# Kernel tuning notes

Hardware: AMD Instinct MI355X
Metric: run time of the kernel (lower is better)

The kernel has to match this reference:

```python
import jax, jax.numpy as jnp
import numpy as np

B, IN, H, T = 512, 256, 128, 100

def _build_norm_adj():
    # Hardcoded topology from GraphConvLSTM.build_graph (22 nodes, cliques per sublist)
    adj_list = [[0, 2, 5, 8, 11], [0, 1, 4, 7, 10], [0, 3, 6, 9, 12, 15],
                [9, 14, 17, 19, 21], [9, 13, 16, 18, 20]]
    n = max(max(s) for s in adj_list) + 1  # 22
    A = np.zeros((n, n), dtype=np.float32)
    for s in adj_list:
        for i in range(len(s)):
            for j in range(i + 1, len(s)):
                A[s[i], s[j]] = 1.0
                A[s[j], s[i]] = 1.0
    # DGL GraphConv norm='both': D^{-1/2} A D^{-1/2} (degrees clamped to >=1)
    deg = np.clip(A.sum(axis=1), 1.0, None)
    dinv = 1.0 / np.sqrt(deg)
    return jnp.asarray(dinv[:, None] * A * dinv[None, :])  # (N, N)

A_NORM = _build_norm_adj()
N = A_NORM.shape[0]  # 22

def setup_inputs() -> dict:
    key = jax.random.key(0)
    ks = jax.random.split(key, 11)
    s_in = 1.0 / np.sqrt(IN)
    s_h = 1.0 / np.sqrt(H)
    return {
        "x":     jax.random.normal(ks[0], (B, IN), jnp.float32),
        "wi_w":  jax.random.normal(ks[1], (H, IN), jnp.float32) * s_in,
        "wi_b":  jax.random.normal(ks[2], (H,), jnp.float32) * s_in,
        "wf_w":  jax.random.normal(ks[3], (H, IN), jnp.float32) * s_in,
        "wf_b":  jax.random.normal(ks[4], (H,), jnp.float32) * s_in,
        "wo_w":  jax.random.normal(ks[5], (H, IN), jnp.float32) * s_in,
        "wo_b":  jax.random.normal(ks[6], (H,), jnp.float32) * s_in,
        "wc_w":  jax.random.normal(ks[7], (H, IN), jnp.float32) * s_in,
        "wc_b":  jax.random.normal(ks[8], (H,), jnp.float32) * s_in,
        "gcn_w": jax.random.normal(ks[9], (H, H), jnp.float32) * s_h,
        "gcn_b": jax.random.normal(ks[10], (H,), jnp.float32) * s_h,
    }

def reference(x, wi_w, wi_b, wf_w, wf_b, wo_w, wo_b, wc_w, wc_b, gcn_w, gcn_b):
    # x is fixed across timesteps in the original forward -> project gates once.
    xi = (x @ wi_w.T + wi_b)[:, None, :]  # (B,1,H) broadcast over nodes
    xf = (x @ wf_w.T + wf_b)[:, None, :]
    xo = (x @ wo_w.T + wo_b)[:, None, :]
    xc = (x @ wc_w.T + wc_b)[:, None, :]

    def step(carry, _):
        h, c = carry
        # All four gates share the identical gcn_h(g, h_prev) result.
        msg = jnp.einsum('mn,bnh->bmh', A_NORM, h)  # (B,N,H)
        g = msg @ gcn_w + gcn_b
        i_t = jax.nn.sigmoid(xi + g)
        f_t = jax.nn.sigmoid(xf + g)
        o_t = jax.nn.sigmoid(xo + g)
        c_til = jnp.tanh(xc + g)
        c_t = f_t * c + i_t * c_til
        h_t = o_t * jnp.tanh(c_t)
        return (h_t, c_t), h_t

    h0 = jnp.zeros((B, N, H), x.dtype)
    c0 = jnp.zeros((B, N, H), x.dtype)
    _, hs = jax.lax.scan(step, (h0, c0), None, length=T)  # (T,B,N,H)
    out = jnp.transpose(hs, (1, 0, 2, 3)).reshape(B, -1)  # (B, T*N*H)
    return out
```

## Files before the change

### kernel.cpp

```cpp
#include <hip/hip_runtime.h>
#include <hip/hip_bf16.h>
#include <math.h>


#define B_   512
#define IN_  256
#define H_   128
#define T_   100
#define N_   22
#define NH   (N_ * H_)
#define TNH  (T_ * NH)
#define HP   136
#define THREADS 512
#define LOG2E 1.442695041f

typedef __attribute__((ext_vector_type(8)))  _Float16 half8_t;
typedef __attribute__((ext_vector_type(16))) float    f32x16;

__global__ void __launch_bounds__(THREADS, 4)
gclstm_kernel(const float* __restrict__ x,
              const float* __restrict__ wi_w, const float* __restrict__ wi_b,
              const float* __restrict__ wf_w, const float* __restrict__ wf_b,
              const float* __restrict__ wo_w, const float* __restrict__ wo_b,
              const float* __restrict__ wc_w, const float* __restrict__ wc_b,
              const float* __restrict__ gcn_w, const float* __restrict__ gcn_b,
              float* __restrict__ out)
{
    __shared__ __align__(16) _Float16 h_hi[32][HP];
    __shared__ __align__(16) _Float16 h_lo[32][HP];
    __shared__ __align__(16) float    hw_T[H_ * 32];
    __shared__ float xp_lds[4][H_];
    __shared__ __align__(16) float xrow[IN_];

    const int t     = threadIdx.x;
    const int b     = blockIdx.x;
    const int ho    = t & (H_ - 1);
    const int mg    = t >> 7;
    const int wid   = t >> 6;
    const int lane  = t & 63;
    const int l31   = lane & 31;
    const int khalf = lane >> 5;

    if (t < IN_ / 4) {
        reinterpret_cast<float4*>(xrow)[t] =
            reinterpret_cast<const float4*>(x + (size_t)b * IN_)[t];
    }
    for (int e = t; e < 32 * HP / 2; e += THREADS) ((int*)h_hi)[e] = 0;
    for (int e = t; e < 32 * HP / 2; e += THREADS) ((int*)h_lo)[e] = 0;
    __syncthreads();

    {
        const float* wg = (mg == 0) ? wi_w : (mg == 1) ? wf_w : (mg == 2) ? wo_w : wc_w;
        const float* bg = (mg == 0) ? wi_b : (mg == 1) ? wf_b : (mg == 2) ? wo_b : wc_b;
        const float* rg = wg + (size_t)ho * IN_;
        float acc = bg[ho];
        #pragma unroll
        for (int k4 = 0; k4 < IN_ / 4; ++k4) {
            float4 xv = reinterpret_cast<const float4*>(xrow)[k4];
            float4 wv = reinterpret_cast<const float4*>(rg)[k4];
            acc += wv.x * xv.x + wv.y * xv.y + wv.z * xv.z + wv.w * xv.w;
        }
        xp_lds[mg][ho] = acc;
    }

    half8_t Bf[8];
    if (wid < 4) {
        const int col = 32 * wid + l31;
        #pragma unroll
        for (int kk = 0; kk < 8; ++kk) {
            #pragma unroll
            for (int i = 0; i < 8; ++i) {
                Bf[kk][i] = (_Float16)gcn_w[(16 * kk + 8 * khalf + i) * H_ + col];
            }
        }
    }
    __syncthreads();

    const float gb   = gcn_b[ho];
    const float xi_r = xp_lds[0][ho] + gb;
    const float xf_r = xp_lds[1][ho] + gb;
    const float xo_r = xp_lds[2][ho] + gb;
    const float xc_r = xp_lds[3][ho] + gb;
    const float Ei   = __builtin_exp2f(-LOG2E * xi_r);
    const float Ef   = __builtin_exp2f(-LOG2E * xf_r);
    const float Eo   = __builtin_exp2f(-LOG2E * xo_r);
    const float E2c  = __builtin_exp2f(-2.0f * LOG2E * xc_r);

    float c_reg[6];
    #pragma unroll
    for (int i = 0; i < 6; ++i) c_reg[i] = 0.0f;

    float* outb = out + (size_t)b * TNH + ho;

    #define D13 0.2773500981126146f
    #define D5  0.4472135954999579f
    #define D4  0.5f
    const float DINV[22] = {D13, D4, D4, D5, D4, D4, D5, D4, D4, D13, D4,
                            D4,  D5, D4, D4, D5, D4, D4, D4, D4, D4,  D4};

    for (int step = 0; step < T_; ++step) {
        if (wid < 4) {
            f32x16 acc = (f32x16)(0.0f);
            #pragma unroll
            for (int kk = 0; kk < 8; ++kk) {
                const int ko = 16 * kk + 8 * khalf;
                const half8_t Ah = *reinterpret_cast<const half8_t*>(&h_hi[l31][ko]);
                const half8_t Al = *reinterpret_cast<const half8_t*>(&h_lo[l31][ko]);
                acc = __builtin_amdgcn_mfma_f32_32x32x16_f16(Ah, Bf[kk], acc, 0, 0, 0);
                acc = __builtin_amdgcn_mfma_f32_32x32x16_f16(Al, Bf[kk], acc, 0, 0, 0);
            }
            const int col = 32 * wid + l31;
            #pragma unroll
            for (int q = 0; q < 4; ++q) {
                float4 v = make_float4(acc[4 * q], acc[4 * q + 1],
                                       acc[4 * q + 2], acc[4 * q + 3]);
                const int unit = (2 * q + khalf) ^ (col & 7);
                *reinterpret_cast<float4*>(&hw_T[col * 32 + unit * 4]) = v;
            }
        }
        __syncthreads();

        float tt[24];
        #pragma unroll
        for (int u = 0; u < 6; ++u) {
            const int unit = u ^ (ho & 7);
            float4 v = *reinterpret_cast<const float4*>(&hw_T[ho * 32 + unit * 4]);
            tt[4 * u + 0] = v.x; tt[4 * u + 1] = v.y;
            tt[4 * u + 2] = v.z; tt[4 * u + 3] = v.w;
        }
        #pragma unroll
        for (int m = 0; m < 22; ++m) tt[m] *= DINV[m];

        const float S0 = tt[0] + tt[2] + tt[5] + tt[8] + tt[11];
        const float S1 = tt[0] + tt[1] + tt[4] + tt[7] + tt[10];
        const float S2 = tt[0] + tt[3] + tt[6] + tt[9] + tt[12] + tt[15];
        const float S3 = tt[9] + tt[14] + tt[17] + tt[19] + tt[21];
        const float S4 = tt[9] + tt[13] + tt[16] + tt[18] + tt[20];

        float* outs = outb + (size_t)step * NH;

        #define UPD(n, nn, SSexpr, KK) {                                        \
            const float g   = DINV[n] * ((SSexpr) - (KK) * tt[n]);              \
            const float E   = __builtin_exp2f(-LOG2E * g);                      \
            const float it  = __builtin_amdgcn_rcpf(1.0f + E * Ei);             \
            const float ft  = __builtin_amdgcn_rcpf(1.0f + E * Ef);             \
            const float ot  = __builtin_amdgcn_rcpf(1.0f + E * Eo);             \
            const float e2  = fminf(E * E * E2c, 1e30f);                        \
            const float ct  = (1.0f - e2) * __builtin_amdgcn_rcpf(1.0f + e2);   \
            const float cn  = ft * c_reg[nn] + it * ct;                         \
            c_reg[nn] = cn;                                                     \
            const float e2n = fminf(__builtin_exp2f(-2.0f * LOG2E * cn), 1e30f);\
            const float th  = (1.0f - e2n) * __builtin_amdgcn_rcpf(1.0f + e2n); \
            const float hn  = ot * th;                                          \
            outs[(n) * H_] = hn;                                                \
            const _Float16 hh = (_Float16)hn;                                   \
            h_hi[n][ho] = hh;                                                   \
            h_lo[n][ho] = (_Float16)(hn - (float)hh);                           \
        }

        if (mg == 0) {
            UPD(0, 0, S0 + S1 + S2, 3.0f)
            UPD(1, 1, S1, 1.0f)
            UPD(2, 2, S0, 1.0f)
            UPD(3, 3, S2, 1.0f)
            UPD(4, 4, S1, 1.0f)
            UPD(5, 5, S0, 1.0f)
        } else if (mg == 1) {
            UPD(6, 0, S2, 1.0f)
            UPD(7, 1, S1, 1.0f)
            UPD(8, 2, S0, 1.0f)
            UPD(9, 3, S2 + S3 + S4, 3.0f)
            UPD(10, 4, S1, 1.0f)
        } else if (mg == 2) {
            UPD(11, 0, S0, 1.0f)
            UPD(12, 1, S2, 1.0f)
            UPD(13, 2, S4, 1.0f)
            UPD(14, 3, S3, 1.0f)
            UPD(15, 4, S2, 1.0f)
            UPD(16, 5, S4, 1.0f)
        } else {
            UPD(17, 0, S3, 1.0f)
            UPD(18, 1, S4, 1.0f)
            UPD(19, 2, S3, 1.0f)
            UPD(20, 3, S4, 1.0f)
            UPD(21, 4, S3, 1.0f)
        }
        #undef UPD
        __syncthreads();
    }
}

extern "C" void kernel_launch(void* const* d_in, const int* in_sizes, int n_in,
                              void* d_out, int out_size, void* d_ws, size_t ws_size,
                              hipStream_t stream) {
    const float* x     = (const float*)d_in[0];
    const float* wi_w  = (const float*)d_in[1];
    const float* wi_b  = (const float*)d_in[2];
    const float* wf_w  = (const float*)d_in[3];
    const float* wf_b  = (const float*)d_in[4];
    const float* wo_w  = (const float*)d_in[5];
    const float* wo_b  = (const float*)d_in[6];
    const float* wc_w  = (const float*)d_in[7];
    const float* wc_b  = (const float*)d_in[8];
    const float* gcn_w = (const float*)d_in[9];
    const float* gcn_b = (const float*)d_in[10];
    float* out = (float*)d_out;

    gclstm_kernel<<<dim3(B_), dim3(THREADS), 0, stream>>>(
        x, wi_w, wi_b, wf_w, wf_b, wo_w, wo_b, wc_w, wc_b, gcn_w, gcn_b, out);
}
```

Before: 794.5 us.

## Keep MFMA results in registers and split node updates across half-waves

The block shrinks to 256 threads (four waves), and every wave runs the MFMA for its 32 output columns. The hi and lo products now go into two separate accumulators, which gives the MFMA chain two independent dependency paths. The results are exchanged between half-waves with a cross-lane shuffle instead of the shared-memory transpose buffer, which removes one barrier and the LDS round trip per step. Each lane then updates 11 nodes instead of 5-6, so per-thread serial transcendental work grows and twice as many blocks can share a CU.

```diff
diff --git a/kernel.cpp b/kernel.cpp
--- a/kernel.cpp
+++ b/kernel.cpp
@@ -11,13 +11,17 @@
 #define NH   (N_ * H_)
 #define TNH  (T_ * NH)
 #define HP   136
-#define THREADS 512
+#define THREADS 256
 #define LOG2E 1.442695041f
 
 typedef __attribute__((ext_vector_type(8)))  _Float16 half8_t;
 typedef __attribute__((ext_vector_type(16))) float    f32x16;
 
-__global__ void __launch_bounds__(THREADS, 4)
+#define D13 0.2773500981126146f
+#define D5  0.4472135954999579f
+#define D4  0.5f
+
+__global__ void __launch_bounds__(THREADS, 2)
 gclstm_kernel(const float* __restrict__ x,
               const float* __restrict__ wi_w, const float* __restrict__ wi_b,
               const float* __restrict__ wf_w, const float* __restrict__ wf_b,
@@ -28,18 +32,17 @@
 {
     __shared__ __align__(16) _Float16 h_hi[32][HP];
     __shared__ __align__(16) _Float16 h_lo[32][HP];
-    __shared__ __align__(16) float    hw_T[H_ * 32];
     __shared__ float xp_lds[4][H_];
     __shared__ __align__(16) float xrow[IN_];
 
     const int t     = threadIdx.x;
     const int b     = blockIdx.x;
-    const int ho    = t & (H_ - 1);
-    const int mg    = t >> 7;
+    const int lane  = t & 63;
     const int wid   = t >> 6;
-    const int lane  = t & 63;
     const int l31   = lane & 31;
     const int khalf = lane >> 5;
+    const bool k0   = (khalf == 0);
+    const int col   = 32 * wid + l31;
 
     if (t < IN_ / 4) {
         reinterpret_cast<float4*>(xrow)[t] =
@@ -50,97 +53,102 @@
     __syncthreads();
 
     {
-        const float* wg = (mg == 0) ? wi_w : (mg == 1) ? wf_w : (mg == 2) ? wo_w : wc_w;
-        const float* bg = (mg == 0) ? wi_b : (mg == 1) ? wf_b : (mg == 2) ? wo_b : wc_b;
-        const float* rg = wg + (size_t)ho * IN_;
-        float acc = bg[ho];
+        const int ho2 = t & (H_ - 1);
+        const int mg2 = t >> 7;
+        const float* wA = mg2 ? wf_w : wi_w;  const float* bA = mg2 ? wf_b : wi_b;
+        const float* wB = mg2 ? wc_w : wo_w;  const float* bB = mg2 ? wc_b : wo_b;
+        const float* rA = wA + (size_t)ho2 * IN_;
+        const float* rB = wB + (size_t)ho2 * IN_;
+        float accA = bA[ho2], accB = bB[ho2];
         #pragma unroll
         for (int k4 = 0; k4 < IN_ / 4; ++k4) {
             float4 xv = reinterpret_cast<const float4*>(xrow)[k4];
-            float4 wv = reinterpret_cast<const float4*>(rg)[k4];
-            acc += wv.x * xv.x + wv.y * xv.y + wv.z * xv.z + wv.w * xv.w;
-        }
-        xp_lds[mg][ho] = acc;
+            float4 wv = reinterpret_cast<const float4*>(rA)[k4];
+            accA += wv.x * xv.x + wv.y * xv.y + wv.z * xv.z + wv.w * xv.w;
+            float4 uv = reinterpret_cast<const float4*>(rB)[k4];
+            accB += uv.x * xv.x + uv.y * xv.y + uv.z * xv.z + uv.w * xv.w;
+        }
+        xp_lds[mg2][ho2]     = accA;
+        xp_lds[mg2 + 2][ho2] = accB;
     }
 
     half8_t Bf[8];
-    if (wid < 4) {
-        const int col = 32 * wid + l31;
+    #pragma unroll
+    for (int kk = 0; kk < 8; ++kk) {
+        #pragma unroll
+        for (int i = 0; i < 8; ++i) {
+            Bf[kk][i] = (_Float16)gcn_w[(16 * kk + 8 * khalf + i) * H_ + col];
+        }
+    }
+    __syncthreads();
+
+    const float gb  = gcn_b[col];
+    const float Ei  = __builtin_exp2f(-LOG2E * (xp_lds[0][col] + gb));
+    const float Ef  = __builtin_exp2f(-LOG2E * (xp_lds[1][col] + gb));
+    const float Eo  = __builtin_exp2f(-LOG2E * (xp_lds[2][col] + gb));
+    const float E2c = __builtin_exp2f(-2.0f * LOG2E * (xp_lds[3][col] + gb));
+
+    const float A1_0 = k0 ? D13 : D4;  const float A2_0 = k0 ? 3.0f * D13 : D4;
+    const float A1_1 = k0 ? D4 : D5;
+    const float A1_3 = k0 ? D5 : D4;
+    const float A1_4 = k0 ? D4 : D5;
+    const float A1_6 = k0 ? D5 : D4;
+    const float A1_9 = k0 ? D13 : D4;  const float A2_9 = k0 ? 3.0f * D13 : D4;
+
+    float c_reg[11];
+    #pragma unroll
+    for (int i = 0; i < 11; ++i) c_reg[i] = 0.0f;
+
+    const int nb = k0 ? 0 : 11;
+    _Float16* hhp = &h_hi[0][0] + nb * HP + col;
+    _Float16* hlp = &h_lo[0][0] + nb * HP + col;
+    float* outb = out + (size_t)b * TNH + nb * H_ + col;
+
+    for (int step = 0; step < T_; ++step) {
+        f32x16 accA = (f32x16)(0.0f);
+        f32x16 accB = (f32x16)(0.0f);
         #pragma unroll
         for (int kk = 0; kk < 8; ++kk) {
-            #pragma unroll
-            for (int i = 0; i < 8; ++i) {
-                Bf[kk][i] = (_Float16)gcn_w[(16 * kk + 8 * khalf + i) * H_ + col];
-            }
-        }
-    }
-    __syncthreads();
-
-    const float gb   = gcn_b[ho];
-    const float xi_r = xp_lds[0][ho] + gb;
-    const float xf_r = xp_lds[1][ho] + gb;
-    const float xo_r = xp_lds[2][ho] + gb;
-    const float xc_r = xp_lds[3][ho] + gb;
-    const float Ei   = __builtin_exp2f(-LOG2E * xi_r);
-    const float Ef   = __builtin_exp2f(-LOG2E * xf_r);
-    const float Eo   = __builtin_exp2f(-LOG2E * xo_r);
-    const float E2c  = __builtin_exp2f(-2.0f * LOG2E * xc_r);
-
-    float c_reg[6];
-    #pragma unroll
-    for (int i = 0; i < 6; ++i) c_reg[i] = 0.0f;
-
-    float* outb = out + (size_t)b * TNH + ho;
-
-    #define D13 0.2773500981126146f
-    #define D5  0.4472135954999579f
-    #define D4  0.5f
-    const float DINV[22] = {D13, D4, D4, D5, D4, D4, D5, D4, D4, D13, D4,
-                            D4,  D5, D4, D4, D5, D4, D4, D4, D4, D4,  D4};
-
-    for (int step = 0; step < T_; ++step) {
-        if (wid < 4) {
-            f32x16 acc = (f32x16)(0.0f);
-            #pragma unroll
-            for (int kk = 0; kk < 8; ++kk) {
-                const int ko = 16 * kk + 8 * khalf;
-                const half8_t Ah = *reinterpret_cast<const half8_t*>(&h_hi[l31][ko]);
-                const half8_t Al = *reinterpret_cast<const half8_t*>(&h_lo[l31][ko]);
-                acc = __builtin_amdgcn_mfma_f32_32x32x16_f16(Ah, Bf[kk], acc, 0, 0, 0);
-                acc = __builtin_amdgcn_mfma_f32_32x32x16_f16(Al, Bf[kk], acc, 0, 0, 0);
-            }
-            const int col = 32 * wid + l31;
-            #pragma unroll
-            for (int q = 0; q < 4; ++q) {
-                float4 v = make_float4(acc[4 * q], acc[4 * q + 1],
-                                       acc[4 * q + 2], acc[4 * q + 3]);
-                const int unit = (2 * q + khalf) ^ (col & 7);
-                *reinterpret_cast<float4*>(&hw_T[col * 32 + unit * 4]) = v;
-            }
-        }
-        __syncthreads();
-
-        float tt[24];
-        #pragma unroll
-        for (int u = 0; u < 6; ++u) {
-            const int unit = u ^ (ho & 7);
-            float4 v = *reinterpret_cast<const float4*>(&hw_T[ho * 32 + unit * 4]);
-            tt[4 * u + 0] = v.x; tt[4 * u + 1] = v.y;
-            tt[4 * u + 2] = v.z; tt[4 * u + 3] = v.w;
-        }
-        #pragma unroll
-        for (int m = 0; m < 22; ++m) tt[m] *= DINV[m];
-
-        const float S0 = tt[0] + tt[2] + tt[5] + tt[8] + tt[11];
-        const float S1 = tt[0] + tt[1] + tt[4] + tt[7] + tt[10];
-        const float S2 = tt[0] + tt[3] + tt[6] + tt[9] + tt[12] + tt[15];
-        const float S3 = tt[9] + tt[14] + tt[17] + tt[19] + tt[21];
-        const float S4 = tt[9] + tt[13] + tt[16] + tt[18] + tt[20];
+            const int ko = 16 * kk + 8 * khalf;
+            const half8_t Ah = *reinterpret_cast<const half8_t*>(&h_hi[l31][ko]);
+            const half8_t Al = *reinterpret_cast<const half8_t*>(&h_lo[l31][ko]);
+            accA = __builtin_amdgcn_mfma_f32_32x32x16_f16(Ah, Bf[kk], accA, 0, 0, 0);
+            accB = __builtin_amdgcn_mfma_f32_32x32x16_f16(Al, Bf[kk], accB, 0, 0, 0);
+        }
+        float hw[12];
+        #pragma unroll
+        for (int s = 0; s < 12; ++s) hw[s] = accA[s] + accB[s];
+
+        float oth[12];
+        #pragma unroll
+        for (int s = 0; s < 12; ++s) oth[s] = __shfl_xor(hw[s], 32, 64);
+        float sel0[12], sel1[10];
+        #pragma unroll
+        for (int s = 0; s < 12; ++s) sel0[s] = k0 ? hw[s] : oth[s];
+        #pragma unroll
+        for (int s = 0; s < 10; ++s) sel1[s] = k0 ? oth[s] : hw[s];
+
+        const float tt0  = sel0[0] * D13, tt1  = sel0[1] * D4, tt2  = sel0[2] * D4;
+        const float tt3  = sel0[3] * D5,  tt4  = sel1[0] * D4, tt5  = sel1[1] * D4;
+        const float tt6  = sel1[2] * D5,  tt7  = sel1[3] * D4, tt8  = sel0[4] * D4;
+        const float tt9  = sel0[5] * D13, tt10 = sel0[6] * D4, tt11 = sel0[7] * D4;
+        const float tt12 = sel1[4] * D5,  tt13 = sel1[5] * D4, tt14 = sel1[6] * D4;
+        const float tt15 = sel1[7] * D5,  tt16 = sel0[8] * D4, tt17 = sel0[9] * D4;
+        const float tt18 = sel0[10] * D4, tt19 = sel0[11] * D4;
+        const float tt20 = sel1[8] * D4,  tt21 = sel1[9] * D4;
+
+        const float S0 = tt0 + tt2 + tt5 + tt8 + tt11;
+        const float S1 = tt0 + tt1 + tt4 + tt7 + tt10;
+        const float S2 = tt0 + tt3 + tt6 + tt9 + tt12 + tt15;
+        const float S3 = tt9 + tt14 + tt17 + tt19 + tt21;
+        const float S4 = tt9 + tt13 + tt16 + tt18 + tt20;
+        const float SAB = S0 + S1 + S2;
+        const float SCD = S2 + S3 + S4;
 
         float* outs = outb + (size_t)step * NH;
 
-        #define UPD(n, nn, SSexpr, KK) {                                        \
-            const float g   = DINV[n] * ((SSexpr) - (KK) * tt[n]);              \
+        #define UPD(nn, A1v, A2v, SSv, TMYv) {                                  \
+            const float g   = (A1v) * (SSv) - (A2v) * (TMYv);                   \
             const float E   = __builtin_exp2f(-LOG2E * g);                      \
             const float it  = __builtin_amdgcn_rcpf(1.0f + E * Ei);             \
             const float ft  = __builtin_amdgcn_rcpf(1.0f + E * Ef);             \
@@ -152,40 +160,25 @@
             const float e2n = fminf(__builtin_exp2f(-2.0f * LOG2E * cn), 1e30f);\
             const float th  = (1.0f - e2n) * __builtin_amdgcn_rcpf(1.0f + e2n); \
             const float hn  = ot * th;                                          \
-            outs[(n) * H_] = hn;                                                \
+            outs[(nn) * H_] = hn;                                               \
             const _Float16 hh = (_Float16)hn;                                   \
-            h_hi[n][ho] = hh;                                                   \
-            h_lo[n][ho] = (_Float16)(hn - (float)hh);                           \
-        }
-
-        if (mg == 0) {
-            UPD(0, 0, S0 + S1 + S2, 3.0f)
-            UPD(1, 1, S1, 1.0f)
-            UPD(2, 2, S0, 1.0f)
-            UPD(3, 3, S2, 1.0f)
-            UPD(4, 4, S1, 1.0f)
-            UPD(5, 5, S0, 1.0f)
-        } else if (mg == 1) {
-            UPD(6, 0, S2, 1.0f)
-            UPD(7, 1, S1, 1.0f)
-            UPD(8, 2, S0, 1.0f)
-            UPD(9, 3, S2 + S3 + S4, 3.0f)
-            UPD(10, 4, S1, 1.0f)
-        } else if (mg == 2) {
-            UPD(11, 0, S0, 1.0f)
-            UPD(12, 1, S2, 1.0f)
-            UPD(13, 2, S4, 1.0f)
-            UPD(14, 3, S3, 1.0f)
-            UPD(15, 4, S2, 1.0f)
-            UPD(16, 5, S4, 1.0f)
-        } else {
-            UPD(17, 0, S3, 1.0f)
-            UPD(18, 1, S4, 1.0f)
-            UPD(19, 2, S3, 1.0f)
-            UPD(20, 3, S4, 1.0f)
-            UPD(21, 4, S3, 1.0f)
-        }
+            hhp[(nn) * HP] = hh;                                                \
+            hlp[(nn) * HP] = (_Float16)(hn - (float)hh);                        \
+        }
+
+        UPD(0,  A1_0, A2_0, k0 ? SAB : S0, k0 ? tt0  : tt11)
+        UPD(1,  A1_1, A1_1, k0 ? S1  : S2, k0 ? tt1  : tt12)
+        UPD(2,  D4,   D4,   k0 ? S0  : S4, k0 ? tt2  : tt13)
+        UPD(3,  A1_3, A1_3, k0 ? S2  : S3, k0 ? tt3  : tt14)
+        UPD(4,  A1_4, A1_4, k0 ? S1  : S2, k0 ? tt4  : tt15)
+        UPD(5,  D4,   D4,   k0 ? S0  : S4, k0 ? tt5  : tt16)
+        UPD(6,  A1_6, A1_6, k0 ? S2  : S3, k0 ? tt6  : tt17)
+        UPD(7,  D4,   D4,   k0 ? S1  : S4, k0 ? tt7  : tt18)
+        UPD(8,  D4,   D4,   k0 ? S0  : S3, k0 ? tt8  : tt19)
+        UPD(9,  A1_9, A2_9, k0 ? SCD : S4, k0 ? tt9  : tt20)
+        UPD(10, D4,   D4,   k0 ? S1  : S3, k0 ? tt10 : tt21)
         #undef UPD
+
         __syncthreads();
     }
 }
```

After: 808.7 us. Within noise of the previous version (+1.8%).

## Apply graph aggregation via second MFMA instead of scalar clique sums

Applied to the files above, without the earlier changes.

Instead of computing per-node clique sums S0..S4 with scalar adds and DINV scaling after the H×W product, the kernel builds the normalized adjacency in LDS and does the node aggregation as a second MFMA stage. Partial results are exchanged with cross-lane shuffles and split into hi/lo fp16. The gate math is also restructured to share one reciprocal across the three sigmoids, and the h·W split accumulation now uses two independent accumulators. This moves scalar VALU work onto the matrix units and shortens the dependency chains. The cost is extra MFMAs, shuffles and fp16 split conversions, plus some precision risk from the split products and the removed clamps.

```diff
diff --git a/kernel.cpp b/kernel.cpp
--- a/kernel.cpp
+++ b/kernel.cpp
@@ -16,6 +16,14 @@
 
 typedef __attribute__((ext_vector_type(8)))  _Float16 half8_t;
 typedef __attribute__((ext_vector_type(16))) float    f32x16;
+
+#define D13 0.2773500981126146f
+#define D5  0.4472135954999579f
+#define D4  0.5f
+
+__device__ __forceinline__ float dinv_of(int i) {
+    return (i == 0 || i == 9) ? D13 : ((i == 3 || i == 6 || i == 12 || i == 15) ? D5 : D4);
+}
 
 __global__ void __launch_bounds__(THREADS, 4)
 gclstm_kernel(const float* __restrict__ x,
@@ -28,18 +36,21 @@
 {
     __shared__ __align__(16) _Float16 h_hi[32][HP];
     __shared__ __align__(16) _Float16 h_lo[32][HP];
-    __shared__ __align__(16) float    hw_T[H_ * 32];
+    __shared__ __align__(16) float    G_T[H_ * 32];
+    __shared__ __align__(16) float    A_lds[32][32];
     __shared__ float xp_lds[4][H_];
     __shared__ __align__(16) float xrow[IN_];
 
     const int t     = threadIdx.x;
     const int b     = blockIdx.x;
-    const int ho    = t & (H_ - 1);
-    const int mg    = t >> 7;
+    const int lane  = t & 63;
     const int wid   = t >> 6;
-    const int lane  = t & 63;
     const int l31   = lane & 31;
     const int khalf = lane >> 5;
+    const bool k0   = (khalf == 0);
+    const int colW  = 32 * (wid & 3) + l31;
+    const int col2  = t & (H_ - 1);
+    const int q     = t >> 7;
 
     if (t < IN_ / 4) {
         reinterpret_cast<float4*>(xrow)[t] =
@@ -47,145 +58,169 @@
     }
     for (int e = t; e < 32 * HP / 2; e += THREADS) ((int*)h_hi)[e] = 0;
     for (int e = t; e < 32 * HP / 2; e += THREADS) ((int*)h_lo)[e] = 0;
+    for (int e = t; e < 32 * 32; e += THREADS) ((float*)A_lds)[e] = 0.0f;
     __syncthreads();
 
     {
-        const float* wg = (mg == 0) ? wi_w : (mg == 1) ? wf_w : (mg == 2) ? wo_w : wc_w;
-        const float* bg = (mg == 0) ? wi_b : (mg == 1) ? wf_b : (mg == 2) ? wo_b : wc_b;
-        const float* rg = wg + (size_t)ho * IN_;
-        float acc = bg[ho];
+        const float* wg = (q == 0) ? wi_w : (q == 1) ? wf_w : (q == 2) ? wo_w : wc_w;
+        const float* bg = (q == 0) ? wi_b : (q == 1) ? wf_b : (q == 2) ? wo_b : wc_b;
+        const float* rg = wg + (size_t)col2 * IN_;
+        float acc = bg[col2];
         #pragma unroll
         for (int k4 = 0; k4 < IN_ / 4; ++k4) {
             float4 xv = reinterpret_cast<const float4*>(xrow)[k4];
             float4 wv = reinterpret_cast<const float4*>(rg)[k4];
             acc += wv.x * xv.x + wv.y * xv.y + wv.z * xv.z + wv.w * xv.w;
         }
-        xp_lds[mg][ho] = acc;
-    }
-
-    half8_t Bf[8];
+        xp_lds[q][col2] = acc;
+    }
+
+    if (t < N_ * N_) {
+        const unsigned int masks[5] = {2341u, 1171u, 37449u, 2769408u, 1384960u};
+        const int i = t / N_, j = t % N_;
+        bool adj = false;
+        if (i != j) {
+            #pragma unroll
+            for (int c = 0; c < 5; ++c)
+                adj |= (((masks[c] >> i) & 1u) != 0u) && (((masks[c] >> j) & 1u) != 0u);
+        }
+        if (adj) A_lds[i][j] = dinv_of(i) * dinv_of(j);
+    }
+    __syncthreads();
+
+    half8_t Wf[8];
+    half8_t AtH[2], AtL[2];
     if (wid < 4) {
-        const int col = 32 * wid + l31;
         #pragma unroll
-        for (int kk = 0; kk < 8; ++kk) {
+        for (int kk = 0; kk < 8; ++kk)
+            #pragma unroll
+            for (int i = 0; i < 8; ++i)
+                Wf[kk][i] = (_Float16)gcn_w[(16 * kk + 8 * khalf + i) * H_ + colW];
+        #pragma unroll
+        for (int kt = 0; kt < 2; ++kt)
             #pragma unroll
             for (int i = 0; i < 8; ++i) {
-                Bf[kk][i] = (_Float16)gcn_w[(16 * kk + 8 * khalf + i) * H_ + col];
-            }
-        }
-    }
-    __syncthreads();
-
-    const float gb   = gcn_b[ho];
-    const float xi_r = xp_lds[0][ho] + gb;
-    const float xf_r = xp_lds[1][ho] + gb;
-    const float xo_r = xp_lds[2][ho] + gb;
-    const float xc_r = xp_lds[3][ho] + gb;
-    const float Ei   = __builtin_exp2f(-LOG2E * xi_r);
-    const float Ef   = __builtin_exp2f(-LOG2E * xf_r);
-    const float Eo   = __builtin_exp2f(-LOG2E * xo_r);
-    const float E2c  = __builtin_exp2f(-2.0f * LOG2E * xc_r);
+                const float a = A_lds[l31][16 * kt + 8 * khalf + i];
+                const _Float16 ah = (_Float16)a;
+                AtH[kt][i] = ah;
+                AtL[kt][i] = (_Float16)(a - (float)ah);
+            }
+    }
+
+    const float gb  = gcn_b[col2];
+    const float Ei  = __builtin_exp2f(-LOG2E * (xp_lds[0][col2] + gb));
+    const float Ef  = __builtin_exp2f(-LOG2E * (xp_lds[1][col2] + gb));
+    const float Eo  = __builtin_exp2f(-LOG2E * (xp_lds[2][col2] + gb));
+    const float E2c = __builtin_exp2f(-2.0f * LOG2E * (xp_lds[3][col2] + gb));
 
     float c_reg[6];
     #pragma unroll
     for (int i = 0; i < 6; ++i) c_reg[i] = 0.0f;
 
-    float* outb = out + (size_t)b * TNH + ho;
-
-    #define D13 0.2773500981126146f
-    #define D5  0.4472135954999579f
-    #define D4  0.5f
-    const float DINV[22] = {D13, D4, D4, D5, D4, D4, D5, D4, D4, D13, D4,
-                            D4,  D5, D4, D4, D5, D4, D4, D4, D4, D4,  D4};
+    float* outb = out + (size_t)b * TNH + col2;
+    const int swW = colW & 7;
+    const int sw2 = col2 & 7;
 
     for (int step = 0; step < T_; ++step) {
         if (wid < 4) {
-            f32x16 acc = (f32x16)(0.0f);
+            f32x16 accA = (f32x16)(0.0f);
+            f32x16 accB = (f32x16)(0.0f);
             #pragma unroll
             for (int kk = 0; kk < 8; ++kk) {
                 const int ko = 16 * kk + 8 * khalf;
                 const half8_t Ah = *reinterpret_cast<const half8_t*>(&h_hi[l31][ko]);
                 const half8_t Al = *reinterpret_cast<const half8_t*>(&h_lo[l31][ko]);
-                acc = __builtin_amdgcn_mfma_f32_32x32x16_f16(Ah, Bf[kk], acc, 0, 0, 0);
-                acc = __builtin_amdgcn_mfma_f32_32x32x16_f16(Al, Bf[kk], acc, 0, 0, 0);
-            }
-            const int col = 32 * wid + l31;
-            #pragma unroll
-            for (int q = 0; q < 4; ++q) {
-                float4 v = make_float4(acc[4 * q], acc[4 * q + 1],
-                                       acc[4 * q + 2], acc[4 * q + 3]);
-                const int unit = (2 * q + khalf) ^ (col & 7);
-                *reinterpret_cast<float4*>(&hw_T[col * 32 + unit * 4]) = v;
+                accA = __builtin_amdgcn_mfma_f32_32x32x16_f16(Ah, Wf[kk], accA, 0, 0, 0);
+                accB = __builtin_amdgcn_mfma_f32_32x32x16_f16(Al, Wf[kk], accB, 0, 0, 0);
+            }
+            float y[12], z[12];
+            #pragma unroll
+            for (int s = 0; s < 12; ++s) y[s] = accA[s] + accB[s];
+            #pragma unroll
+            for (int s = 0; s < 12; ++s) z[s] = __shfl_xor(y[s], 32, 64);
+
+            float ba[8], bb[8];
+            #pragma unroll
+            for (int i = 0; i < 4; ++i) {
+                ba[i]     = k0 ? y[i]     : z[4 + i];
+                ba[4 + i] = k0 ? z[i]     : y[4 + i];
+                bb[i]     = y[8 + i];
+                bb[4 + i] = z[8 + i];
+            }
+            half8_t BaH, BaL, BbH, BbL;
+            #pragma unroll
+            for (int i = 0; i < 8; ++i) {
+                const _Float16 h1 = (_Float16)ba[i];
+                BaH[i] = h1;  BaL[i] = (_Float16)(ba[i] - (float)h1);
+                const _Float16 h2 = (_Float16)bb[i];
+                BbH[i] = h2;  BbL[i] = (_Float16)(bb[i] - (float)h2);
+            }
+            f32x16 gA = (f32x16)(0.0f);
+            gA = __builtin_amdgcn_mfma_f32_32x32x16_f16(AtH[0], BaH, gA, 0, 0, 0);
+            gA = __builtin_amdgcn_mfma_f32_32x32x16_f16(AtH[1], BbH, gA, 0, 0, 0);
+            gA = __builtin_amdgcn_mfma_f32_32x32x16_f16(AtH[0], BaL, gA, 0, 0, 0);
+            gA = __builtin_amdgcn_mfma_f32_32x32x16_f16(AtH[1], BbL, gA, 0, 0, 0);
+            gA = __builtin_amdgcn_mfma_f32_32x32x16_f16(AtL[0], BaH, gA, 0, 0, 0);
+            gA = __builtin_amdgcn_mfma_f32_32x32x16_f16(AtL[1], BbH, gA, 0, 0, 0);
+
+            #pragma unroll
+            for (int qq = 0; qq < 3; ++qq) {
+                float4 v = make_float4(gA[4 * qq], gA[4 * qq + 1],
+                                       gA[4 * qq + 2], gA[4 * qq + 3]);
+                const int unit = (2 * qq + khalf) ^ swW;
+                *reinterpret_cast<float4*>(&G_T[colW * 32 + unit * 4]) = v;
             }
         }
         __syncthreads();
 
-        float tt[24];
-        #pragma unroll
-        for (int u = 0; u < 6; ++u) {
-            const int unit = u ^ (ho & 7);
-            float4 v = *reinterpret_cast<const float4*>(&hw_T[ho * 32 + unit * 4]);
-            tt[4 * u + 0] = v.x; tt[4 * u + 1] = v.y;
-            tt[4 * u + 2] = v.z; tt[4 * u + 3] = v.w;
-        }
-        #pragma unroll
-        for (int m = 0; m < 22; ++m) tt[m] *= DINV[m];
-
-        const float S0 = tt[0] + tt[2] + tt[5] + tt[8] + tt[11];
-        const float S1 = tt[0] + tt[1] + tt[4] + tt[7] + tt[10];
-        const float S2 = tt[0] + tt[3] + tt[6] + tt[9] + tt[12] + tt[15];
-        const float S3 = tt[9] + tt[14] + tt[17] + tt[19] + tt[21];
-        const float S4 = tt[9] + tt[13] + tt[16] + tt[18] + tt[20];
+        int UA, UB;
+        if      (q == 0) { UA = 0; UB = 1; }
+        else if (q == 1) { UA = 1; UB = 2; }
+        else if (q == 2) { UA = 2; UB = 3; }
+        else             { UA = 4; UB = 5; }
+        const float4 va = *reinterpret_cast<const float4*>(&G_T[col2 * 32 + ((UA ^ sw2) << 2)]);
+        const float4 vb = *reinterpret_cast<const float4*>(&G_T[col2 * 32 + ((UB ^ sw2) << 2)]);
 
         float* outs = outb + (size_t)step * NH;
 
-        #define UPD(n, nn, SSexpr, KK) {                                        \
-            const float g   = DINV[n] * ((SSexpr) - (KK) * tt[n]);              \
-            const float E   = __builtin_exp2f(-LOG2E * g);                      \
-            const float it  = __builtin_amdgcn_rcpf(1.0f + E * Ei);             \
-            const float ft  = __builtin_amdgcn_rcpf(1.0f + E * Ef);             \
-            const float ot  = __builtin_amdgcn_rcpf(1.0f + E * Eo);             \
-            const float e2  = fminf(E * E * E2c, 1e30f);                        \
-            const float ct  = (1.0f - e2) * __builtin_amdgcn_rcpf(1.0f + e2);   \
-            const float cn  = ft * c_reg[nn] + it * ct;                         \
-            c_reg[nn] = cn;                                                     \
-            const float e2n = fminf(__builtin_exp2f(-2.0f * LOG2E * cn), 1e30f);\
-            const float th  = (1.0f - e2n) * __builtin_amdgcn_rcpf(1.0f + e2n); \
-            const float hn  = ot * th;                                          \
+        #define UPDN(n, sl, gval) {                                             \
+            const float E  = __builtin_exp2f(-LOG2E * (gval));                  \
+            const float u  = __builtin_fmaf(E, Ei, 1.0f);                       \
+            const float v  = __builtin_fmaf(E, Ef, 1.0f);                       \
+            const float w  = __builtin_fmaf(E, Eo, 1.0f);                       \
+            const float uv = u * v, vw = v * w, uw = u * w;                     \
+            const float rP = __builtin_amdgcn_rcpf(uv * w);                     \
+            const float it = vw * rP, ft = uw * rP, ot = uv * rP;               \
+            const float e2 = E * E * E2c;                                       \
+            const float ct = __builtin_fmaf(2.0f,                               \
+                                __builtin_amdgcn_rcpf(1.0f + e2), -1.0f);       \
+            const float cn = __builtin_fmaf(ft, c_reg[sl], it * ct);            \
+            c_reg[sl] = cn;                                                     \
+            const float en = __builtin_exp2f((2.0f * LOG2E) * cn);              \
+            const float th = __builtin_fmaf(-2.0f,                              \
+                                __builtin_amdgcn_rcpf(1.0f + en), 1.0f);        \
+            const float hn = ot * th;                                           \
             outs[(n) * H_] = hn;                                                \
             const _Float16 hh = (_Float16)hn;                                   \
-            h_hi[n][ho] = hh;                                                   \
-            h_lo[n][ho] = (_Float16)(hn - (float)hh);                           \
-        }
-
-        if (mg == 0) {
-            UPD(0, 0, S0 + S1 + S2, 3.0f)
-            UPD(1, 1, S1, 1.0f)
-            UPD(2, 2, S0, 1.0f)
-            UPD(3, 3, S2, 1.0f)
-            UPD(4, 4, S1, 1.0f)
-            UPD(5, 5, S0, 1.0f)
-        } else if (mg == 1) {
-            UPD(6, 0, S2, 1.0f)
-            UPD(7, 1, S1, 1.0f)
-            UPD(8, 2, S0, 1.0f)
-            UPD(9, 3, S2 + S3 + S4, 3.0f)
-            UPD(10, 4, S1, 1.0f)
-        } else if (mg == 2) {
-            UPD(11, 0, S0, 1.0f)
-            UPD(12, 1, S2, 1.0f)
-            UPD(13, 2, S4, 1.0f)
-            UPD(14, 3, S3, 1.0f)
-            UPD(15, 4, S2, 1.0f)
-            UPD(16, 5, S4, 1.0f)
+            h_hi[n][col2] = hh;                                                 \
+            h_lo[n][col2] = (_Float16)(hn - (float)hh);                         \
+        }
+
+        if (q == 0) {
+            UPDN(0, 0, va.x) UPDN(1, 1, va.y) UPDN(2, 2, va.z)
+            UPDN(3, 3, va.w) UPDN(4, 4, vb.x) UPDN(5, 5, vb.y)
+        } else if (q == 1) {
+            UPDN(6, 0, va.z) UPDN(7, 1, va.w) UPDN(8, 2, vb.x)
+            UPDN(9, 3, vb.y) UPDN(10, 4, vb.z)
+        } else if (q == 2) {
+            UPDN(11, 0, va.w) UPDN(12, 1, vb.x) UPDN(13, 2, vb.y)
+            UPDN(14, 3, vb.z) UPDN(15, 4, vb.w)
         } else {
-            UPD(17, 0, S3, 1.0f)
-            UPD(18, 1, S4, 1.0f)
-            UPD(19, 2, S3, 1.0f)
-            UPD(20, 3, S4, 1.0f)
-            UPD(21, 4, S3, 1.0f)
-        }
-        #undef UPD
+            UPDN(16, 0, va.x) UPDN(17, 1, va.y) UPDN(18, 2, va.z)
+            UPDN(19, 3, va.w) UPDN(20, 4, vb.x) UPDN(21, 5, vb.y)
+        }
+        #undef UPDN
+
         __syncthreads();
     }
 }
```

Measured after the change: 813.2 us. +2.4%, slower.
